# Performance work log

Measured on AMD Instinct MI355X. Metric: run time of the kernel, lower is better.

## Reference

```python
import jax, jax.numpy as jnp
import numpy as np

EMBED = 512  # scale uses embed_size**-0.5 per the original forward (NOT head_size)


def setup_inputs() -> dict:
    key = jax.random.key(0)
    k1, k2, k3, k4 = jax.random.split(key, 4)
    B, T, D, H = 8, 4096, EMBED, 64
    inputs = jax.random.normal(k1, (B, T, D), dtype=jnp.float32)
    Wq = jax.random.normal(k2, (D, H), dtype=jnp.float32) * (D ** -0.5)
    Wk = jax.random.normal(k3, (D, H), dtype=jnp.float32) * (D ** -0.5)
    Wv = jax.random.normal(k4, (D, H), dtype=jnp.float32) * (D ** -0.5)
    return {"inputs": inputs, "Wq": Wq, "Wk": Wk, "Wv": Wv}


def reference(inputs, Wq, Wk, Wv):
    # inputs: [B, T, D]; Wq/Wk/Wv: [D, H]
    B, T, D = inputs.shape
    q = inputs @ Wq  # [B, T, H]
    k = inputs @ Wk  # [B, T, H]
    v = inputs @ Wv  # [B, T, H]
    scale = jnp.asarray(D, inputs.dtype) ** -0.5  # original scales by embed_size**-0.5
    scores = jnp.einsum('bth,bsh->bts', q, k) * scale  # [B, T, T]
    causal = jnp.arange(T)[:, None] >= jnp.arange(T)[None, :]  # lower-triangular
    scores = jnp.where(causal, scores, jnp.asarray(-jnp.inf, scores.dtype))
    weights = jax.nn.softmax(scores, axis=-1)
    # dropout is identity in eval mode
    return weights @ v  # [B, T, H]
```

## Files before the change

kernel.cpp:

```cpp
#include <hip/hip_runtime.h>
#include <hip/hip_bf16.h>
#include <math.h>

#define TSEQ 4096
#define NB 8
#define DEM 512
#define HD 64
#define LP 72
#define WIP 136
#define WIMG 26624
#define QSZ ((size_t)NB * TSEQ * HD)
#define SLOTS_PER_B 144

typedef __attribute__((ext_vector_type(8))) short short8;
typedef __attribute__((ext_vector_type(4))) short short4v;
typedef __attribute__((ext_vector_type(4))) float float4v;

__device__ __forceinline__ short f2bf(float f) {
    union { float f; unsigned u; } v; v.f = f;
    unsigned r = v.u + 0x7fffu + ((v.u >> 16) & 1u);
    return (short)(r >> 16);
}

__device__ __forceinline__ short8 pack8(float4 a, float4 b) {
    union { short8 s; __hip_bfloat162 h[4]; } u;
    u.h[0] = __float22bfloat162_rn(make_float2(a.x, a.y));
    u.h[1] = __float22bfloat162_rn(make_float2(a.z, a.w));
    u.h[2] = __float22bfloat162_rn(make_float2(b.x, b.y));
    u.h[3] = __float22bfloat162_rn(make_float2(b.z, b.w));
    return u.s;
}

__device__ __forceinline__ void gload_lds16(const void* g, void* l) {
    __builtin_amdgcn_global_load_lds(
        (const __attribute__((address_space(1))) unsigned int*)g,
        (__attribute__((address_space(3))) unsigned int*)l,
        16, 0, 0);
}

__device__ __host__ __forceinline__ int slot_base(int mq) {
    int a = mq >> 2, r = mq & 3;
    return (a + 1) * (2 * a + r);
}

__global__ __launch_bounds__(256) void wtr_kernel(
    const float* __restrict__ Wq, const float* __restrict__ Wk,
    const float* __restrict__ Wv, short* __restrict__ wimg)
{
    __shared__ float t[64][65];
    const int tid = threadIdx.x;
    const int kb = blockIdx.x;
    const int k0 = kb * 64;
    const int m = blockIdx.y;
    const int c = kb >> 1, half = kb & 1;
    const float* W = (m == 0) ? Wq : ((m == 1) ? Wk : Wv);
    const float sc = (m == 0) ? 0.044194173824159216f : 1.0f;

#pragma unroll
    for (int i = 0; i < 4; ++i) {
        int f = tid + 256 * i;
        int k = f >> 4, n4 = (f & 15) * 4;
        float4 wv = *(const float4*)&W[(k0 + k) * HD + n4];
        t[k][n4 + 0] = wv.x; t[k][n4 + 1] = wv.y;
        t[k][n4 + 2] = wv.z; t[k][n4 + 3] = wv.w;
    }
    __syncthreads();
#pragma unroll
    for (int i = 0; i < 4; ++i) {
        int f = tid + 256 * i;
        int n = f >> 4, k4 = (f & 15) * 4;
        short4v o;
        o[0] = f2bf(t[k4 + 0][n] * sc);
        o[1] = f2bf(t[k4 + 1][n] * sc);
        o[2] = f2bf(t[k4 + 2][n] * sc);
        o[3] = f2bf(t[k4 + 3][n] * sc);
        *(short4v*)&wimg[c * WIMG + (64 * m + n) * WIP + half * 64 + k4] = o;
    }
}

__global__ __launch_bounds__(256, 2) void qkv_mfma(
    const float* __restrict__ x, const short* __restrict__ wimg,
    short* __restrict__ q, short* __restrict__ k, short* __restrict__ vt)
{
    __shared__ alignas(16) short wlds[WIMG];

    const int tid = threadIdx.x;
    const int w = tid >> 6;
    const int l15 = tid & 15;
    const int quad = (tid >> 4) & 3;
    const int rbase = blockIdx.x * 64 + w * 16 + l15;

    const float* xr = x + (size_t)rbase * DEM;
    float4v acc[12] = {};

    for (int c = 0; c < 4; ++c) {
        __syncthreads();
        {
            const char* gsrc = (const char*)(wimg + c * WIMG) + tid * 16;
            char* ldst = (char*)wlds + tid * 16;
#pragma unroll
            for (int i = 0; i < 13; ++i)
                gload_lds16(gsrc + i * 4096, ldst + i * 4096);
        }
        __syncthreads();

#pragma unroll
        for (int ks = 0; ks < 4; ++ks) {
            const int k0 = c * 128 + ks * 32 + quad * 8;
            float4 xa = *(const float4*)&xr[k0];
            float4 xb = *(const float4*)&xr[k0 + 4];
            short8 xv = pack8(xa, xb);
            const int lk = ks * 32 + quad * 8;
#pragma unroll
            for (int mt = 0; mt < 12; ++mt) {
                short8 wf = *(const short8*)&wlds[(mt * 16 + l15) * WIP + lk];
                acc[mt] = __builtin_amdgcn_mfma_f32_16x16x32_bf16(wf, xv, acc[mt], 0, 0, 0);
            }
        }
    }

#pragma unroll
    for (int mt = 0; mt < 8; ++mt) {
        short* dst = (mt < 4) ? q : k;
        short4v o;
        o[0] = f2bf(acc[mt][0]); o[1] = f2bf(acc[mt][1]);
        o[2] = f2bf(acc[mt][2]); o[3] = f2bf(acc[mt][3]);
        *(short4v*)&dst[(size_t)rbase * HD + (mt & 3) * 16 + quad * 4] = o;
    }
    const int b = rbase >> 12, t = rbase & (TSEQ - 1);
#pragma unroll
    for (int mt = 8; mt < 12; ++mt) {
#pragma unroll
        for (int reg = 0; reg < 4; ++reg) {
            int d = (mt - 8) * 16 + quad * 4 + reg;
            vt[((size_t)(b * HD + d)) * TSEQ + t] = f2bf(acc[mt][reg]);
        }
    }
}

__global__ __launch_bounds__(256, 4) void flash_mfma(
    const short* __restrict__ qw, const short* __restrict__ kw,
    const short* __restrict__ vtw, float* __restrict__ out,
    float* __restrict__ pO, float* __restrict__ stS)
{
    __shared__ short kt[64 * LP];
    __shared__ short vt[64 * LP];
    __shared__ short pt[4][32 * LP];

    const int tid = threadIdx.x;
    const int w = tid >> 6;
    const int l15 = tid & 15;
    const int quad = (tid >> 4) & 3;
    const int bx = blockIdx.x;
    const int b = bx & 7;
    const int idx = bx >> 3;

    int mq, j;
    if (idx < 120) {
        int t = idx;
        mq = 31; j = 0;
#pragma unroll 1
        for (int mm = 31; mm >= 3; --mm) {
            int f = (mm + 1) >> 2;
            if (t < f) { mq = mm; j = t; break; }
            t -= f;
        }
    } else {
        int t = idx - 120;
        int kc = t >> 3, p = t & 7;
        mq = (30 - kc) - 4 * p;
        j = (mq + 1) >> 2;
    }
    const int s0 = 8 * j;
    const int send = min(8 * (j + 1), 2 * mq + 2);
    const int r0 = mq * 128;
    const int slot = b * SLOTS_PER_B + slot_base(mq) + j;

    short8 qf[2][2];
#pragma unroll
    for (int g = 0; g < 2; ++g) {
        const short* qrow = qw + ((size_t)(b * TSEQ + r0 + 32 * w + 16 * g + l15)) * HD;
        qf[g][0] = *(const short8*)(qrow + quad * 8);
        qf[g][1] = *(const short8*)(qrow + 32 + quad * 8);
    }

    float l_lane[2] = {0.f, 0.f};
    float4v O[2][4] = {};

    const int srow = tid >> 3, sc = tid & 7;
    const short* kbase = kw + (size_t)b * TSEQ * HD;
    const short* vbase = vtw + (size_t)b * HD * TSEQ;

    short8 kr0, kr1, vr0, vr1;
    {
        const short* kg = kbase + (size_t)(s0 * 64) * HD;
        const short* vg = vbase + s0 * 64;
        kr0 = *(const short8*)(kg + srow * HD + sc * 8);
        kr1 = *(const short8*)(kg + (srow + 32) * HD + sc * 8);
        vr0 = *(const short8*)(vg + (size_t)srow * TSEQ + sc * 8);
        vr1 = *(const short8*)(vg + (size_t)(srow + 32) * TSEQ + sc * 8);
    }

    for (int st = s0; st < send; ++st) {
        __syncthreads();
        *(short8*)&kt[srow * LP + sc * 8] = kr0;
        *(short8*)&kt[(srow + 32) * LP + sc * 8] = kr1;
        *(short8*)&vt[srow * LP + sc * 8] = vr0;
        *(short8*)&vt[(srow + 32) * LP + sc * 8] = vr1;
        __syncthreads();

        if (st + 1 < send) {
            const short* kg = kbase + (size_t)((st + 1) * 64) * HD;
            const short* vg = vbase + (st + 1) * 64;
            kr0 = *(const short8*)(kg + srow * HD + sc * 8);
            kr1 = *(const short8*)(kg + (srow + 32) * HD + sc * 8);
            vr0 = *(const short8*)(vg + (size_t)srow * TSEQ + sc * 8);
            vr1 = *(const short8*)(vg + (size_t)(srow + 32) * TSEQ + sc * 8);
        }

        float4v S[2][4] = {};
        __builtin_amdgcn_s_setprio(1);
#pragma unroll
        for (int mt = 0; mt < 4; ++mt) {
            short8 a0 = *(const short8*)&kt[(mt * 16 + l15) * LP + quad * 8];
            short8 a1 = *(const short8*)&kt[(mt * 16 + l15) * LP + 32 + quad * 8];
            S[0][mt] = __builtin_amdgcn_mfma_f32_16x16x32_bf16(a0, qf[0][0], S[0][mt], 0, 0, 0);
            S[0][mt] = __builtin_amdgcn_mfma_f32_16x16x32_bf16(a1, qf[0][1], S[0][mt], 0, 0, 0);
            S[1][mt] = __builtin_amdgcn_mfma_f32_16x16x32_bf16(a0, qf[1][0], S[1][mt], 0, 0, 0);
            S[1][mt] = __builtin_amdgcn_mfma_f32_16x16x32_bf16(a1, qf[1][1], S[1][mt], 0, 0, 0);
        }
        __builtin_amdgcn_s_setprio(0);

        if (st >= 2 * mq) {
            const int kb2 = st * 64;
#pragma unroll
            for (int g = 0; g < 2; ++g) {
                int qg = r0 + 32 * w + 16 * g + l15;
#pragma unroll
                for (int mt = 0; mt < 4; ++mt)
#pragma unroll
                    for (int r = 0; r < 4; ++r)
                        if (kb2 + mt * 16 + quad * 4 + r > qg) S[g][mt][r] = -INFINITY;
            }
        }

#pragma unroll
        for (int g = 0; g < 2; ++g) {
#pragma unroll
            for (int mt = 0; mt < 4; ++mt) {
                float p0 = __expf(S[g][mt][0]);
                float p1 = __expf(S[g][mt][1]);
                float p2 = __expf(S[g][mt][2]);
                float p3 = __expf(S[g][mt][3]);
                l_lane[g] += (p0 + p1) + (p2 + p3);
                union { short4v s; __hip_bfloat162 h[2]; } pk;
                pk.h[0] = __float22bfloat162_rn(make_float2(p0, p1));
                pk.h[1] = __float22bfloat162_rn(make_float2(p2, p3));
                *(short4v*)&pt[w][(16 * g + l15) * LP + mt * 16 + quad * 4] = pk.s;
            }
        }

        __builtin_amdgcn_s_setprio(1);
#pragma unroll
        for (int kf = 0; kf < 2; ++kf) {
            short8 pa0 = *(const short8*)&pt[w][l15 * LP + kf * 32 + quad * 8];
            short8 pa1 = *(const short8*)&pt[w][(16 + l15) * LP + kf * 32 + quad * 8];
#pragma unroll
            for (int nt = 0; nt < 4; ++nt) {
                short8 vb = *(const short8*)&vt[(nt * 16 + l15) * LP + kf * 32 + quad * 8];
                O[0][nt] = __builtin_amdgcn_mfma_f32_16x16x32_bf16(pa0, vb, O[0][nt], 0, 0, 0);
                O[1][nt] = __builtin_amdgcn_mfma_f32_16x16x32_bf16(pa1, vb, O[1][nt], 0, 0, 0);
            }
        }
        __builtin_amdgcn_s_setprio(0);
    }

    float lred[2];
#pragma unroll
    for (int g = 0; g < 2; ++g) {
        float rs = l_lane[g];
        rs += __shfl_xor(rs, 16, 64);
        rs += __shfl_xor(rs, 32, 64);
        lred[g] = rs;
    }

    if (mq <= 3) {
#pragma unroll
        for (int g = 0; g < 2; ++g) {
            float iv = 1.0f / lred[g];
#pragma unroll
            for (int r = 0; r < 4; ++r) {
                float ir = __shfl(iv, quad * 4 + r, 64);
                size_t row = (size_t)(b * TSEQ + r0 + 32 * w + 16 * g + quad * 4 + r) * HD;
#pragma unroll
                for (int nt = 0; nt < 4; ++nt)
                    out[row + nt * 16 + l15] = O[g][nt][r] * ir;
            }
        }
    } else {
        float* dest = pO + (size_t)slot * 128 * HD;
#pragma unroll
        for (int g = 0; g < 2; ++g) {
#pragma unroll
            for (int r = 0; r < 4; ++r) {
                size_t row = (size_t)(32 * w + 16 * g + quad * 4 + r) * HD;
#pragma unroll
                for (int nt = 0; nt < 4; ++nt)
                    dest[row + nt * 16 + l15] = O[g][nt][r];
            }
            if (quad == 0) stS[slot * 128 + 32 * w + 16 * g + l15] = lred[g];
        }
    }
}

__global__ __launch_bounds__(256) void merge_kernel(
    float* __restrict__ out, const float* __restrict__ pO,
    const float* __restrict__ stS)
{
    const int tid = threadIdx.x;
    const int bx = blockIdx.x;
    const int b = bx / 56, loc = bx - b * 56;
    const int t = 512 + loc * 64 + (tid >> 2);
    const int dq = (tid & 3) * 16;
    const int mq = t >> 7, rr = t & 127;
    const int nseg = (mq + 4) >> 2;
    const int sb = b * SLOTS_PER_B + slot_base(mq);

    float denom = 0.f;
    for (int s = 0; s < nseg; ++s) denom += stS[(sb + s) * 128 + rr];
    float inv = 1.0f / denom;

    float4 o[4] = {};
    for (int s = 0; s < nseg; ++s) {
        const float4* pp = (const float4*)
            &pO[((size_t)(sb + s) * 128 + rr) * HD + dq];
#pragma unroll
        for (int i = 0; i < 4; ++i) {
            float4 p = pp[i];
            o[i].x += p.x; o[i].y += p.y;
            o[i].z += p.z; o[i].w += p.w;
        }
    }
    float4* op = (float4*)&out[((size_t)b * TSEQ + t) * HD + dq];
#pragma unroll
    for (int i = 0; i < 4; ++i) {
        o[i].x *= inv; o[i].y *= inv; o[i].z *= inv; o[i].w *= inv;
        op[i] = o[i];
    }
}

extern "C" void kernel_launch(void* const* d_in, const int* in_sizes, int n_in,
                              void* d_out, int out_size, void* d_ws, size_t ws_size,
                              hipStream_t stream) {
    const float* x  = (const float*)d_in[0];
    const float* Wq = (const float*)d_in[1];
    const float* Wk = (const float*)d_in[2];
    const float* Wv = (const float*)d_in[3];
    float* out = (float*)d_out;

    short* q  = (short*)d_ws;
    short* k  = q + QSZ;
    short* vt = k + QSZ;
    short* wimg = vt + QSZ;
    float* pO = (float*)(wimg + 4 * WIMG);
    float* stS = pO + (size_t)NB * SLOTS_PER_B * 128 * HD;

    wtr_kernel<<<dim3(8, 3), 256, 0, stream>>>(Wq, Wk, Wv, wimg);
    qkv_mfma<<<dim3(NB * TSEQ / 64), 256, 0, stream>>>(x, wimg, q, k, vt);
    flash_mfma<<<dim3(NB * SLOTS_PER_B), 256, 0, stream>>>(q, k, vt, out, pO, stS);
    merge_kernel<<<dim3(448), 256, 0, stream>>>(out, pO, stS);
}
```

Baseline: 161.4 us.

## Split flash attention into single-wave blocks using 32x32x16 MFMA with register P

Each 256-thread workgroup handling 128 query rows becomes four independent 64-thread workgroups of 32 rows each, iterating over 32-key tiles. QK^T and PV now use the 32x32x16 bf16 MFMA. The P matrix stays in registers via lane shuffles instead of round-tripping through LDS, and each wave stops at its own causal bound, skipping fully masked tiles. K/V tiles are no longer shared across four waves, so global/L2 traffic for K and V rises about fourfold, and each wave issues more loads per tile.

```diff
diff --git a/kernel.cpp b/kernel.cpp
--- a/kernel.cpp
+++ b/kernel.cpp
@@ -6,7 +6,8 @@
 #define NB 8
 #define DEM 512
 #define HD 64
-#define LP 72
+#define KP 66
+#define VP 34
 #define WIP 136
 #define WIMG 26624
 #define QSZ ((size_t)NB * TSEQ * HD)
@@ -15,6 +16,7 @@
 typedef __attribute__((ext_vector_type(8))) short short8;
 typedef __attribute__((ext_vector_type(4))) short short4v;
 typedef __attribute__((ext_vector_type(4))) float float4v;
+typedef __attribute__((ext_vector_type(16))) float f32x16;
 
 __device__ __forceinline__ short f2bf(float f) {
     union { float f; unsigned u; } v; v.f = f;
@@ -28,6 +30,18 @@
     u.h[1] = __float22bfloat162_rn(make_float2(a.z, a.w));
     u.h[2] = __float22bfloat162_rn(make_float2(b.x, b.y));
     u.h[3] = __float22bfloat162_rn(make_float2(b.z, b.w));
+    return u.s;
+}
+
+__device__ __forceinline__ int pkbf2(float x, float y) {
+    union { __hip_bfloat162 h; int i; } u;
+    u.h = __float22bfloat162_rn(make_float2(x, y));
+    return u.i;
+}
+
+__device__ __forceinline__ short8 mk8(int a, int b, int c, int d) {
+    union { short8 s; int i[4]; } u;
+    u.i[0] = a; u.i[1] = b; u.i[2] = c; u.i[3] = d;
     return u.s;
 }
 
@@ -138,22 +152,22 @@
     }
 }
 
-__global__ __launch_bounds__(256, 4) void flash_mfma(
+__global__ __launch_bounds__(64, 3) void flash_mfma(
     const short* __restrict__ qw, const short* __restrict__ kw,
     const short* __restrict__ vtw, float* __restrict__ out,
     float* __restrict__ pO, float* __restrict__ stS)
 {
-    __shared__ short kt[64 * LP];
-    __shared__ short vt[64 * LP];
-    __shared__ short pt[4][32 * LP];
-
-    const int tid = threadIdx.x;
-    const int w = tid >> 6;
-    const int l15 = tid & 15;
-    const int quad = (tid >> 4) & 3;
+    __shared__ short kt[32 * KP];
+    __shared__ short vl[64 * VP];
+
+    const int lane = threadIdx.x;
+    const int q5 = lane & 31;
+    const int hi = lane >> 5;
     const int bx = blockIdx.x;
     const int b = bx & 7;
-    const int idx = bx >> 3;
+    const int r = bx >> 3;
+    const int w = r & 3;
+    const int idx = r >> 2;
 
     int mq, j;
     if (idx < 120) {
@@ -171,145 +185,133 @@
         mq = (30 - kc) - 4 * p;
         j = (mq + 1) >> 2;
     }
-    const int s0 = 8 * j;
-    const int send = min(8 * (j + 1), 2 * mq + 2);
     const int r0 = mq * 128;
+    const int ss0 = 16 * j;
+    const int ssend = min(16 * (j + 1), 4 * mq + w + 1);
     const int slot = b * SLOTS_PER_B + slot_base(mq) + j;
-
-    short8 qf[2][2];
-#pragma unroll
-    for (int g = 0; g < 2; ++g) {
-        const short* qrow = qw + ((size_t)(b * TSEQ + r0 + 32 * w + 16 * g + l15)) * HD;
-        qf[g][0] = *(const short8*)(qrow + quad * 8);
-        qf[g][1] = *(const short8*)(qrow + 32 + quad * 8);
-    }
-
-    float l_lane[2] = {0.f, 0.f};
-    float4v O[2][4] = {};
-
-    const int srow = tid >> 3, sc = tid & 7;
+    const int qrow = r0 + w * 32 + q5;
+
+    short8 qf[4];
+    {
+        const short* qp = qw + ((size_t)(b * TSEQ + qrow)) * HD + hi * 8;
+#pragma unroll
+        for (int ks = 0; ks < 4; ++ks) qf[ks] = *(const short8*)(qp + ks * 16);
+    }
+
+    f32x16 O0 = {}, O1 = {};
+    float l_lane = 0.f;
+
     const short* kbase = kw + (size_t)b * TSEQ * HD;
     const short* vbase = vtw + (size_t)b * HD * TSEQ;
-
-    short8 kr0, kr1, vr0, vr1;
+    const int krow = lane >> 3, kc8 = (lane & 7) * 8;
+    const int vrow = lane >> 2, vc8 = (lane & 3) * 8;
+
+    short8 pk0, pk1, pk2, pk3, pv0, pv1, pv2, pv3;
     {
-        const short* kg = kbase + (size_t)(s0 * 64) * HD;
-        const short* vg = vbase + s0 * 64;
-        kr0 = *(const short8*)(kg + srow * HD + sc * 8);
-        kr1 = *(const short8*)(kg + (srow + 32) * HD + sc * 8);
-        vr0 = *(const short8*)(vg + (size_t)srow * TSEQ + sc * 8);
-        vr1 = *(const short8*)(vg + (size_t)(srow + 32) * TSEQ + sc * 8);
-    }
-
-    for (int st = s0; st < send; ++st) {
+        const short* kg = kbase + (size_t)(ss0 * 32) * HD;
+        const short* vg = vbase + ss0 * 32;
+        pk0 = *(const short8*)(kg + (krow +  0) * HD + kc8);
+        pk1 = *(const short8*)(kg + (krow +  8) * HD + kc8);
+        pk2 = *(const short8*)(kg + (krow + 16) * HD + kc8);
+        pk3 = *(const short8*)(kg + (krow + 24) * HD + kc8);
+        pv0 = *(const short8*)(vg + (size_t)(vrow +  0) * TSEQ + vc8);
+        pv1 = *(const short8*)(vg + (size_t)(vrow + 16) * TSEQ + vc8);
+        pv2 = *(const short8*)(vg + (size_t)(vrow + 32) * TSEQ + vc8);
+        pv3 = *(const short8*)(vg + (size_t)(vrow + 48) * TSEQ + vc8);
+    }
+
+    for (int ss = ss0; ss < ssend; ++ss) {
         __syncthreads();
-        *(short8*)&kt[srow * LP + sc * 8] = kr0;
-        *(short8*)&kt[(srow + 32) * LP + sc * 8] = kr1;
-        *(short8*)&vt[srow * LP + sc * 8] = vr0;
-        *(short8*)&vt[(srow + 32) * LP + sc * 8] = vr1;
+        *(short8*)&kt[(krow +  0) * KP + kc8] = pk0;
+        *(short8*)&kt[(krow +  8) * KP + kc8] = pk1;
+        *(short8*)&kt[(krow + 16) * KP + kc8] = pk2;
+        *(short8*)&kt[(krow + 24) * KP + kc8] = pk3;
+        *(short8*)&vl[(vrow +  0) * VP + vc8] = pv0;
+        *(short8*)&vl[(vrow + 16) * VP + vc8] = pv1;
+        *(short8*)&vl[(vrow + 32) * VP + vc8] = pv2;
+        *(short8*)&vl[(vrow + 48) * VP + vc8] = pv3;
         __syncthreads();
 
-        if (st + 1 < send) {
-            const short* kg = kbase + (size_t)((st + 1) * 64) * HD;
-            const short* vg = vbase + (st + 1) * 64;
-            kr0 = *(const short8*)(kg + srow * HD + sc * 8);
-            kr1 = *(const short8*)(kg + (srow + 32) * HD + sc * 8);
-            vr0 = *(const short8*)(vg + (size_t)srow * TSEQ + sc * 8);
-            vr1 = *(const short8*)(vg + (size_t)(srow + 32) * TSEQ + sc * 8);
-        }
-
-        float4v S[2][4] = {};
-        __builtin_amdgcn_s_setprio(1);
-#pragma unroll
-        for (int mt = 0; mt < 4; ++mt) {
-            short8 a0 = *(const short8*)&kt[(mt * 16 + l15) * LP + quad * 8];
-            short8 a1 = *(const short8*)&kt[(mt * 16 + l15) * LP + 32 + quad * 8];
-            S[0][mt] = __builtin_amdgcn_mfma_f32_16x16x32_bf16(a0, qf[0][0], S[0][mt], 0, 0, 0);
-            S[0][mt] = __builtin_amdgcn_mfma_f32_16x16x32_bf16(a1, qf[0][1], S[0][mt], 0, 0, 0);
-            S[1][mt] = __builtin_amdgcn_mfma_f32_16x16x32_bf16(a0, qf[1][0], S[1][mt], 0, 0, 0);
-            S[1][mt] = __builtin_amdgcn_mfma_f32_16x16x32_bf16(a1, qf[1][1], S[1][mt], 0, 0, 0);
-        }
-        __builtin_amdgcn_s_setprio(0);
-
-        if (st >= 2 * mq) {
-            const int kb2 = st * 64;
-#pragma unroll
-            for (int g = 0; g < 2; ++g) {
-                int qg = r0 + 32 * w + 16 * g + l15;
-#pragma unroll
-                for (int mt = 0; mt < 4; ++mt)
-#pragma unroll
-                    for (int r = 0; r < 4; ++r)
-                        if (kb2 + mt * 16 + quad * 4 + r > qg) S[g][mt][r] = -INFINITY;
+        if (ss + 1 < ssend) {
+            const short* kg = kbase + (size_t)((ss + 1) * 32) * HD;
+            const short* vg = vbase + (ss + 1) * 32;
+            pk0 = *(const short8*)(kg + (krow +  0) * HD + kc8);
+            pk1 = *(const short8*)(kg + (krow +  8) * HD + kc8);
+            pk2 = *(const short8*)(kg + (krow + 16) * HD + kc8);
+            pk3 = *(const short8*)(kg + (krow + 24) * HD + kc8);
+            pv0 = *(const short8*)(vg + (size_t)(vrow +  0) * TSEQ + vc8);
+            pv1 = *(const short8*)(vg + (size_t)(vrow + 16) * TSEQ + vc8);
+            pv2 = *(const short8*)(vg + (size_t)(vrow + 32) * TSEQ + vc8);
+            pv3 = *(const short8*)(vg + (size_t)(vrow + 48) * TSEQ + vc8);
+        }
+
+        f32x16 S = {};
+#pragma unroll
+        for (int ks = 0; ks < 4; ++ks) {
+            short8 a = *(const short8*)&kt[q5 * KP + ks * 16 + hi * 8];
+            S = __builtin_amdgcn_mfma_f32_32x32x16_bf16(a, qf[ks], S, 0, 0, 0);
+        }
+
+        if (ss * 32 + 31 > r0 + w * 32) {
+#pragma unroll
+            for (int reg = 0; reg < 16; ++reg) {
+                int key = ss * 32 + (reg & 3) + 8 * (reg >> 2) + 4 * hi;
+                if (key > qrow) S[reg] = -INFINITY;
             }
         }
 
-#pragma unroll
-        for (int g = 0; g < 2; ++g) {
-#pragma unroll
-            for (int mt = 0; mt < 4; ++mt) {
-                float p0 = __expf(S[g][mt][0]);
-                float p1 = __expf(S[g][mt][1]);
-                float p2 = __expf(S[g][mt][2]);
-                float p3 = __expf(S[g][mt][3]);
-                l_lane[g] += (p0 + p1) + (p2 + p3);
-                union { short4v s; __hip_bfloat162 h[2]; } pk;
-                pk.h[0] = __float22bfloat162_rn(make_float2(p0, p1));
-                pk.h[1] = __float22bfloat162_rn(make_float2(p2, p3));
-                *(short4v*)&pt[w][(16 * g + l15) * LP + mt * 16 + quad * 4] = pk.s;
-            }
-        }
-
-        __builtin_amdgcn_s_setprio(1);
-#pragma unroll
-        for (int kf = 0; kf < 2; ++kf) {
-            short8 pa0 = *(const short8*)&pt[w][l15 * LP + kf * 32 + quad * 8];
-            short8 pa1 = *(const short8*)&pt[w][(16 + l15) * LP + kf * 32 + quad * 8];
-#pragma unroll
-            for (int nt = 0; nt < 4; ++nt) {
-                short8 vb = *(const short8*)&vt[(nt * 16 + l15) * LP + kf * 32 + quad * 8];
-                O[0][nt] = __builtin_amdgcn_mfma_f32_16x16x32_bf16(pa0, vb, O[0][nt], 0, 0, 0);
-                O[1][nt] = __builtin_amdgcn_mfma_f32_16x16x32_bf16(pa1, vb, O[1][nt], 0, 0, 0);
-            }
-        }
-        __builtin_amdgcn_s_setprio(0);
-    }
-
-    float lred[2];
-#pragma unroll
-    for (int g = 0; g < 2; ++g) {
-        float rs = l_lane[g];
-        rs += __shfl_xor(rs, 16, 64);
-        rs += __shfl_xor(rs, 32, 64);
-        lred[g] = rs;
-    }
+        float p[16];
+#pragma unroll
+        for (int reg = 0; reg < 16; ++reg) {
+            p[reg] = __expf(S[reg]);
+            l_lane += p[reg];
+        }
+        int dd[4][2];
+#pragma unroll
+        for (int a = 0; a < 4; ++a) {
+            dd[a][0] = pkbf2(p[4 * a + 0], p[4 * a + 1]);
+            dd[a][1] = pkbf2(p[4 * a + 2], p[4 * a + 3]);
+        }
+        int ra0 = __shfl_xor(hi ? dd[0][0] : dd[1][0], 32, 64);
+        int ra1 = __shfl_xor(hi ? dd[0][1] : dd[1][1], 32, 64);
+        int rb0 = __shfl_xor(hi ? dd[2][0] : dd[3][0], 32, 64);
+        int rb1 = __shfl_xor(hi ? dd[2][1] : dd[3][1], 32, 64);
+        short8 PA0 = hi ? mk8(ra0, ra1, dd[1][0], dd[1][1])
+                        : mk8(dd[0][0], dd[0][1], ra0, ra1);
+        short8 PA1 = hi ? mk8(rb0, rb1, dd[3][0], dd[3][1])
+                        : mk8(dd[2][0], dd[2][1], rb0, rb1);
+
+#pragma unroll
+        for (int kr = 0; kr < 2; ++kr) {
+            short8 pa = kr ? PA1 : PA0;
+            short8 v0 = *(const short8*)&vl[(q5)      * VP + kr * 16 + hi * 8];
+            short8 v1 = *(const short8*)&vl[(32 + q5) * VP + kr * 16 + hi * 8];
+            O0 = __builtin_amdgcn_mfma_f32_32x32x16_bf16(pa, v0, O0, 0, 0, 0);
+            O1 = __builtin_amdgcn_mfma_f32_32x32x16_bf16(pa, v1, O1, 0, 0, 0);
+        }
+    }
+
+    const float ltot = l_lane + __shfl_xor(l_lane, 32, 64);
 
     if (mq <= 3) {
-#pragma unroll
-        for (int g = 0; g < 2; ++g) {
-            float iv = 1.0f / lred[g];
-#pragma unroll
-            for (int r = 0; r < 4; ++r) {
-                float ir = __shfl(iv, quad * 4 + r, 64);
-                size_t row = (size_t)(b * TSEQ + r0 + 32 * w + 16 * g + quad * 4 + r) * HD;
-#pragma unroll
-                for (int nt = 0; nt < 4; ++nt)
-                    out[row + nt * 16 + l15] = O[g][nt][r] * ir;
-            }
+        float inv = 1.0f / ltot;
+#pragma unroll
+        for (int reg = 0; reg < 16; ++reg) {
+            int qloc = (reg & 3) + 8 * (reg >> 2) + 4 * hi;
+            float ir = __shfl(inv, qloc, 64);
+            size_t rowb = (size_t)(b * TSEQ + r0 + w * 32 + qloc) * HD + q5;
+            out[rowb]      = O0[reg] * ir;
+            out[rowb + 32] = O1[reg] * ir;
         }
     } else {
-        float* dest = pO + (size_t)slot * 128 * HD;
-#pragma unroll
-        for (int g = 0; g < 2; ++g) {
-#pragma unroll
-            for (int r = 0; r < 4; ++r) {
-                size_t row = (size_t)(32 * w + 16 * g + quad * 4 + r) * HD;
-#pragma unroll
-                for (int nt = 0; nt < 4; ++nt)
-                    dest[row + nt * 16 + l15] = O[g][nt][r];
-            }
-            if (quad == 0) stS[slot * 128 + 32 * w + 16 * g + l15] = lred[g];
-        }
+        float* dest = pO + ((size_t)slot * 128 + w * 32) * HD + q5;
+#pragma unroll
+        for (int reg = 0; reg < 16; ++reg) {
+            int qloc = (reg & 3) + 8 * (reg >> 2) + 4 * hi;
+            dest[(size_t)qloc * HD]      = O0[reg];
+            dest[(size_t)qloc * HD + 32] = O1[reg];
+        }
+        if (hi == 0) stS[slot * 128 + w * 32 + q5] = ltot;
     }
 }
 
@@ -367,6 +369,6 @@
 
     wtr_kernel<<<dim3(8, 3), 256, 0, stream>>>(Wq, Wk, Wv, wimg);
     qkv_mfma<<<dim3(NB * TSEQ / 64), 256, 0, stream>>>(x, wimg, q, k, vt);
-    flash_mfma<<<dim3(NB * SLOTS_PER_B), 256, 0, stream>>>(q, k, vt, out, pO, stS);
+    flash_mfma<<<dim3(NB * SLOTS_PER_B * 4), 64, 0, stream>>>(q, k, vt, out, pO, stS);
     merge_kernel<<<dim3(448), 256, 0, stream>>>(out, pO, stS);
 }
```

New measurement: 157.7 us. 2.3% less time.
